# Kernel optimization log

Measured on AMD Instinct MI355X. Metric: run time of the kernel, lower is better.

## Reference

```python
import jax, jax.numpy as jnp
import numpy as np

B, S, E, D, A = 32, 2048, 1024, 1024, 1024


def setup_inputs() -> dict:
    key = jax.random.key(0)
    k1, k2, k3, k4, k5, k6, k7, k8 = jax.random.split(key, 8)
    # Kaiming-uniform-ish init scales (values don't matter for correctness)
    def lin(kw, kb, fan_in, fan_out):
        bound = 1.0 / np.sqrt(fan_in)
        W = jax.random.uniform(kw, (fan_out, fan_in), minval=-bound, maxval=bound, dtype=jnp.float32)
        b = jax.random.uniform(kb, (fan_out,), minval=-bound, maxval=bound, dtype=jnp.float32)
        return W, b
    W_enc, b_enc = lin(k1, k2, E, A)
    W_dec, b_dec = lin(k3, k4, D, A)
    W_v, b_v = lin(k5, k6, A, 1)
    encoder_out = jax.random.normal(k7, (B, S, E), dtype=jnp.float32)
    decoder_hidden = jax.random.normal(k8, (B, D), dtype=jnp.float32)
    return {
        "encoder_out": encoder_out,
        "decoder_hidden": decoder_hidden,
        "W_enc": W_enc, "b_enc": b_enc,
        "W_dec": W_dec, "b_dec": b_dec,
        "W_v": W_v, "b_v": b_v,
    }


def reference(encoder_out, decoder_hidden, W_enc, b_enc, W_dec, b_dec, W_v, b_v):
    # encoder_proj: [B, S, A]
    encoder_proj = jnp.einsum('bse,ae->bsa', encoder_out, W_enc) + b_enc
    # decoder_proj: [B, 1, A]
    decoder_proj = (jnp.einsum('bd,ad->ba', decoder_hidden, W_dec) + b_dec)[:, None, :]
    # scores: [B, S] (V projects attention_dim -> 1)
    scores = jnp.einsum('bsa,a->bs', jnp.tanh(encoder_proj + decoder_proj), W_v[0]) + b_v[0]
    alpha = jax.nn.softmax(scores, axis=1)  # [B, S]
    context = jnp.einsum('bse,bs->be', encoder_out, alpha)  # [B, E]
    return (context, alpha)
```

## Files before the change

### kernel.cpp

```cpp
#include <hip/hip_runtime.h>

typedef unsigned short ushort_t;
typedef __attribute__((ext_vector_type(8))) short short8;
typedef __attribute__((ext_vector_type(4))) float f32x4;


__device__ __forceinline__ ushort_t f2bf(float f) {
    unsigned u = __builtin_bit_cast(unsigned, f);
    u += 0x7fffu + ((u >> 16) & 1u);
    return (ushort_t)(u >> 16);
}

__device__ __forceinline__ float bf2f(ushort_t h) {
    unsigned u = ((unsigned)h) << 16;
    return __builtin_bit_cast(float, u);
}

__device__ __forceinline__ float tanh_fast(float x) {
    float e = __expf(2.0f * x);
    float r = __builtin_amdgcn_rcpf(e + 1.0f);
    return __builtin_fmaf(-2.0f, r, 1.0f);
}

__device__ __forceinline__ void gld16(const ushort_t* g, ushort_t* lds) {
    __builtin_amdgcn_global_load_lds(
        (const __attribute__((address_space(1))) unsigned int*)g,
        (__attribute__((address_space(3))) unsigned int*)lds, 16, 0, 0);
}


__global__ __launch_bounds__(256) void k_front(const float* __restrict__ enc,
                                               const float* __restrict__ Wenc,
                                               const float* __restrict__ dh,
                                               const float* __restrict__ Wd,
                                               const float* __restrict__ bd,
                                               const float* __restrict__ be,
                                               ushort_t* __restrict__ encB,
                                               ushort_t* __restrict__ wencB,
                                               float* __restrict__ dproj,
                                               float4* __restrict__ scores4) {
    const int bx = blockIdx.x;
    const int t = threadIdx.x;
    if (bx < 8192) {
        int i = bx * 256 + t;
        for (; i < 17055744; i += 2097152) {
            if (i < 16777216) {
                float4 v = ((const float4*)enc)[i];
                ushort4 o;
                o.x = f2bf(v.x); o.y = f2bf(v.y); o.z = f2bf(v.z); o.w = f2bf(v.w);
                ((ushort4*)encB)[i] = o;
            } else if (i < 17039360) {
                int j = i - 16777216;
                float4 v = ((const float4*)Wenc)[j];
                ushort4 o;
                o.x = f2bf(v.x); o.y = f2bf(v.y); o.z = f2bf(v.z); o.w = f2bf(v.w);
                ((ushort4*)wencB)[j] = o;
            } else {
                scores4[i - 17039360] = (float4){0.f, 0.f, 0.f, 0.f};
            }
        }
    } else {
        int wid = (bx - 8192) * 4 + (t >> 6);
        int lane = t & 63;
        int a = wid & 1023, b = wid >> 10;
        const float4* x = (const float4*)(dh + (size_t)b * 1024);
        const float4* wrow = (const float4*)(Wd + (size_t)a * 1024);
        float s = 0.f;
#pragma unroll
        for (int it = 0; it < 4; ++it) {
            int c = it * 64 + lane;
            float4 xv = x[c], wv = wrow[c];
            s += xv.x * wv.x + xv.y * wv.y + xv.z * wv.z + xv.w * wv.w;
        }
#pragma unroll
        for (int o = 1; o < 64; o <<= 1) s += __shfl_xor(s, o, 64);
        if (lane == 0) dproj[b * 1024 + a] = s + bd[a] + be[a];
    }
}


__global__ __launch_bounds__(256, 2) void k_gemm_scores(const ushort_t* __restrict__ A,
                                                        const ushort_t* __restrict__ Bm,
                                                        const float* __restrict__ dproj,
                                                        const float* __restrict__ Wv,
                                                        float* __restrict__ scores) {
    __shared__ __align__(16) ushort_t At[256 * 64];
    __shared__ __align__(16) ushort_t Bt[128 * 64];

    const int tid = threadIdx.x;
    const int lane = tid & 63;
    const int w = tid >> 6;
    const int wm = w >> 1, wn = w & 1;

    const int blk = blockIdx.x;
    const int q2 = blk >> 3;
    const int blkN = q2 & 7;
    const int blkM = (blk & 7) + ((q2 >> 3) << 3);
    const long long arow0 = (long long)blkM * 256;
    const int brow0 = blkN * 128;

    const int sr = lane >> 3;
    const int sgrp = lane & 7;
    const int c8s = sgrp ^ sr;

    const int q = lane >> 4;
    const int ml = lane & 15;

    const ushort_t* ga = A + (arow0 + w * 64 + sr) * 1024 + c8s * 8;
    const ushort_t* gb = Bm + (long long)(brow0 + w * 32 + sr) * 1024 + c8s * 8;

    f32x4 acc[8][4];
#pragma unroll
    for (int i = 0; i < 8; ++i)
#pragma unroll
        for (int jj = 0; jj < 4; ++jj) acc[i][jj] = (f32x4){0.f, 0.f, 0.f, 0.f};

    for (int k0 = 0; k0 < 1024; k0 += 64) {
        __syncthreads();
#pragma unroll
        for (int j = 0; j < 8; ++j)
            gld16(ga + j * 8192, &At[(w * 8 + j) * 512]);
#pragma unroll
        for (int j = 0; j < 4; ++j)
            gld16(gb + j * 8192, &Bt[(w * 4 + j) * 512]);
        ga += 64; gb += 64;
        __builtin_amdgcn_s_waitcnt(0);
        __syncthreads();

#pragma unroll
        for (int kk = 0; kk < 2; ++kk) {
            const int kb = kk * 4;
            const int slot = (kb + q) ^ (ml & 7);
            short8 af[8], bfr[4];
#pragma unroll
            for (int i = 0; i < 8; ++i) {
                int row = wm * 128 + i * 16 + ml;
                af[i] = *(const short8*)&At[row * 64 + slot * 8];
            }
#pragma unroll
            for (int jj = 0; jj < 4; ++jj) {
                int col = wn * 64 + jj * 16 + ml;
                bfr[jj] = *(const short8*)&Bt[col * 64 + slot * 8];
            }
#pragma unroll
            for (int i = 0; i < 8; ++i)
#pragma unroll
                for (int jj = 0; jj < 4; ++jj)
                    acc[i][jj] = __builtin_amdgcn_mfma_f32_16x16x32_bf16(
                        af[i], bfr[jj], acc[i][jj], 0, 0, 0);
        }
    }

    const int bb = blkM >> 3;
    float dp[4], wv[4];
#pragma unroll
    for (int jj = 0; jj < 4; ++jj) {
        int a = blkN * 128 + wn * 64 + jj * 16 + ml;
        dp[jj] = dproj[bb * 1024 + a];
        wv[jj] = Wv[a];
    }
#pragma unroll
    for (int i = 0; i < 8; ++i) {
        float rs[4] = {0.f, 0.f, 0.f, 0.f};
#pragma unroll
        for (int jj = 0; jj < 4; ++jj) {
            f32x4 v = acc[i][jj];
            rs[0] += wv[jj] * tanh_fast(v.x + dp[jj]);
            rs[1] += wv[jj] * tanh_fast(v.y + dp[jj]);
            rs[2] += wv[jj] * tanh_fast(v.z + dp[jj]);
            rs[3] += wv[jj] * tanh_fast(v.w + dp[jj]);
        }
#pragma unroll
        for (int r = 0; r < 4; ++r)
#pragma unroll
            for (int o = 1; o < 16; o <<= 1) rs[r] += __shfl_xor(rs[r], o, 64);
        if (ml == 0) {
            long long m0 = arow0 + wm * 128 + i * 16 + q * 4;
            atomicAdd(&scores[m0 + 0], rs[0]);
            atomicAdd(&scores[m0 + 1], rs[1]);
            atomicAdd(&scores[m0 + 2], rs[2]);
            atomicAdd(&scores[m0 + 3], rs[3]);
        }
    }
}


__global__ __launch_bounds__(256) void k_softmax(const float* __restrict__ scores,
                                                 float* __restrict__ out) {
    const int b = blockIdx.x, t = threadIdx.x;
    const int lane = t & 63, w = t >> 6;
    __shared__ float red[4];
#pragma unroll
    for (int j = t; j < 1024; j += 256) out[b * 1024 + j] = 0.f;
    float v[8];
#pragma unroll
    for (int j = 0; j < 8; ++j) v[j] = scores[b * 2048 + j * 256 + t];
    float mx = v[0];
#pragma unroll
    for (int j = 1; j < 8; ++j) mx = fmaxf(mx, v[j]);
#pragma unroll
    for (int o = 1; o < 64; o <<= 1) mx = fmaxf(mx, __shfl_xor(mx, o, 64));
    if (lane == 0) red[w] = mx;
    __syncthreads();
    mx = fmaxf(fmaxf(red[0], red[1]), fmaxf(red[2], red[3]));
    float s = 0.f;
#pragma unroll
    for (int j = 0; j < 8; ++j) { v[j] = __expf(v[j] - mx); s += v[j]; }
#pragma unroll
    for (int o = 1; o < 64; o <<= 1) s += __shfl_xor(s, o, 64);
    __syncthreads();
    if (lane == 0) red[w] = s;
    __syncthreads();
    s = red[0] + red[1] + red[2] + red[3];
    float inv = 1.0f / s;
#pragma unroll
    for (int j = 0; j < 8; ++j) out[32768 + b * 2048 + j * 256 + t] = v[j] * inv;
}


__global__ __launch_bounds__(256) void k_context(const ushort_t* __restrict__ encB,
                                                 const float* __restrict__ alpha,
                                                 float* __restrict__ out) {
    const int b = blockIdx.x, ec = blockIdx.y, sc = blockIdx.z, t = threadIdx.x;
    const int l = t & 31, g = t >> 5;
    __shared__ float al[256];
    __shared__ f32x4 part[8][33];
    al[t] = alpha[b * 2048 + sc * 256 + t];
    __syncthreads();
    const ushort_t* ep = encB + ((size_t)(b * 2048 + sc * 256 + g * 32)) * 1024 + ec * 128 + l * 4;
    const float* ag = &al[g * 32];
    f32x4 acc = (f32x4){0.f, 0.f, 0.f, 0.f};
#pragma unroll 4
    for (int s = 0; s < 32; ++s) {
        ushort4 ev = *(const ushort4*)(ep + (size_t)s * 1024);
        float a = ag[s];
        acc.x += a * bf2f(ev.x);
        acc.y += a * bf2f(ev.y);
        acc.z += a * bf2f(ev.z);
        acc.w += a * bf2f(ev.w);
    }
    part[g][l] = acc;
    __syncthreads();
    if (t < 32) {
        f32x4 s = part[0][t];
#pragma unroll
        for (int gg = 1; gg < 8; ++gg) {
            f32x4 p = part[gg][t];
            s.x += p.x; s.y += p.y; s.z += p.z; s.w += p.w;
        }
        float* dst = out + b * 1024 + ec * 128 + t * 4;
        atomicAdd(dst + 0, s.x);
        atomicAdd(dst + 1, s.y);
        atomicAdd(dst + 2, s.z);
        atomicAdd(dst + 3, s.w);
    }
}


extern "C" void kernel_launch(void* const* d_in, const int* in_sizes, int n_in,
                              void* d_out, int out_size, void* d_ws, size_t ws_size,
                              hipStream_t stream) {
    const float* enc  = (const float*)d_in[0];
    const float* dh   = (const float*)d_in[1];
    const float* Wenc = (const float*)d_in[2];
    const float* benc = (const float*)d_in[3];
    const float* Wdec = (const float*)d_in[4];
    const float* bdec = (const float*)d_in[5];
    const float* Wv   = (const float*)d_in[6];
    float* out = (float*)d_out;

    char* ws = (char*)d_ws;
    ushort_t* encB  = (ushort_t*)ws;
    ushort_t* wencB = (ushort_t*)(ws + 134217728ull);
    float* dproj    = (float*)(ws + 134217728ull + 2097152ull);
    float* scores   = (float*)(ws + 134217728ull + 2097152ull + 131072ull);

    k_front<<<16384, 256, 0, stream>>>(enc, Wenc, dh, Wdec, bdec, benc,
                                       encB, wencB, dproj, (float4*)scores);
    k_gemm_scores<<<2048, 256, 0, stream>>>(encB, wencB, dproj, Wv, scores);
    k_softmax<<<32, 256, 0, stream>>>(scores, out);
    k_context<<<dim3(32, 8, 8), 256, 0, stream>>>(encB, out + 32768, out);
}
```

Before: 552.7 us.

## Convert encoder activations to bf16 inside GEMM instead of separate pass

The standalone fp32-to-bf16 conversion of the 256MB encoder tensor is removed. The GEMM now loads fp32 rows directly, packs them to bf16 with v_cvt_pk_bf16_f32 in registers and stores them into LDS, in place of the async global_load_lds for A. The context kernel reads fp32 encoder data directly, with one block per (batch, E-chunk) covering the full sequence, so the output no longer needs atomics or zeroing. This avoids writing and re-reading a 128MB bf16 copy. In exchange the GEMM moves twice the bytes per A tile through registers, and the context kernel reads fp32.

Measured after the change: 608.5 us. +10.1%, slower.

```diff
diff --git a/kernel.cpp b/kernel.cpp
--- a/kernel.cpp
+++ b/kernel.cpp
@@ -3,6 +3,7 @@
 typedef unsigned short ushort_t;
 typedef __attribute__((ext_vector_type(8))) short short8;
 typedef __attribute__((ext_vector_type(4))) float f32x4;
+typedef __attribute__((ext_vector_type(4))) unsigned int u32x4;
 
 
 __device__ __forceinline__ ushort_t f2bf(float f) {
@@ -11,9 +12,10 @@
     return (ushort_t)(u >> 16);
 }
 
-__device__ __forceinline__ float bf2f(ushort_t h) {
-    unsigned u = ((unsigned)h) << 16;
-    return __builtin_bit_cast(float, u);
+__device__ __forceinline__ unsigned pkbf(float a, float b) {
+    unsigned r;
+    asm("v_cvt_pk_bf16_f32 %0, %1, %2" : "=v"(r) : "v"(a), "v"(b));
+    return r;
 }
 
 __device__ __forceinline__ float tanh_fast(float x) {
@@ -29,38 +31,29 @@
 }
 
 
-__global__ __launch_bounds__(256) void k_front(const float* __restrict__ enc,
-                                               const float* __restrict__ Wenc,
-                                               const float* __restrict__ dh,
-                                               const float* __restrict__ Wd,
-                                               const float* __restrict__ bd,
-                                               const float* __restrict__ be,
-                                               ushort_t* __restrict__ encB,
-                                               ushort_t* __restrict__ wencB,
-                                               float* __restrict__ dproj,
-                                               float4* __restrict__ scores4) {
+__global__ __launch_bounds__(256) void k_prep(const float* __restrict__ Wenc,
+                                              const float* __restrict__ dh,
+                                              const float* __restrict__ Wd,
+                                              const float* __restrict__ bd,
+                                              const float* __restrict__ be,
+                                              ushort_t* __restrict__ wencB,
+                                              float* __restrict__ dproj,
+                                              float4* __restrict__ scores4) {
     const int bx = blockIdx.x;
     const int t = threadIdx.x;
-    if (bx < 8192) {
-        int i = bx * 256 + t;
-        for (; i < 17055744; i += 2097152) {
-            if (i < 16777216) {
-                float4 v = ((const float4*)enc)[i];
-                ushort4 o;
-                o.x = f2bf(v.x); o.y = f2bf(v.y); o.z = f2bf(v.z); o.w = f2bf(v.w);
-                ((ushort4*)encB)[i] = o;
-            } else if (i < 17039360) {
-                int j = i - 16777216;
-                float4 v = ((const float4*)Wenc)[j];
-                ushort4 o;
-                o.x = f2bf(v.x); o.y = f2bf(v.y); o.z = f2bf(v.z); o.w = f2bf(v.w);
-                ((ushort4*)wencB)[j] = o;
-            } else {
-                scores4[i - 17039360] = (float4){0.f, 0.f, 0.f, 0.f};
-            }
-        }
+    if (bx < 256) {
+        int idx = bx * 256 + t;
+#pragma unroll
+        for (int r = 0; r < 4; ++r) {
+            int i = idx + r * 65536;
+            float4 v = ((const float4*)Wenc)[i];
+            ushort4 o;
+            o.x = f2bf(v.x); o.y = f2bf(v.y); o.z = f2bf(v.z); o.w = f2bf(v.w);
+            ((ushort4*)wencB)[i] = o;
+        }
+        if (idx < 16384) scores4[idx] = (float4){0.f, 0.f, 0.f, 0.f};
     } else {
-        int wid = (bx - 8192) * 4 + (t >> 6);
+        int wid = (bx - 256) * 4 + (t >> 6);
         int lane = t & 63;
         int a = wid & 1023, b = wid >> 10;
         const float4* x = (const float4*)(dh + (size_t)b * 1024);
@@ -79,7 +72,7 @@
 }
 
 
-__global__ __launch_bounds__(256, 2) void k_gemm_scores(const ushort_t* __restrict__ A,
+__global__ __launch_bounds__(256, 2) void k_gemm_scores(const float* __restrict__ A,
                                                         const ushort_t* __restrict__ Bm,
                                                         const float* __restrict__ dproj,
                                                         const float* __restrict__ Wv,
@@ -106,8 +99,9 @@
     const int q = lane >> 4;
     const int ml = lane & 15;
 
-    const ushort_t* ga = A + (arow0 + w * 64 + sr) * 1024 + c8s * 8;
-    const ushort_t* gb = Bm + (long long)(brow0 + w * 32 + sr) * 1024 + c8s * 8;
+    const float4* ga = (const float4*)(A + (size_t)(arow0 + w * 64 + sr) * 1024) + sgrp * 2;
+    const ushort_t* gb = Bm + (size_t)(brow0 + w * 32 + sr) * 1024 + c8s * 8;
+    const int wls = sr * 64 + (c8s << 3);
 
     f32x4 acc[8][4];
 #pragma unroll
@@ -116,14 +110,29 @@
         for (int jj = 0; jj < 4; ++jj) acc[i][jj] = (f32x4){0.f, 0.f, 0.f, 0.f};
 
     for (int k0 = 0; k0 < 1024; k0 += 64) {
+        float4 p0[4], p1[4];
+#pragma unroll
+        for (int j = 0; j < 4; ++j) { p0[j] = ga[j * 2048]; p1[j] = ga[j * 2048 + 1]; }
         __syncthreads();
-#pragma unroll
-        for (int j = 0; j < 8; ++j)
-            gld16(ga + j * 8192, &At[(w * 8 + j) * 512]);
 #pragma unroll
         for (int j = 0; j < 4; ++j)
             gld16(gb + j * 8192, &Bt[(w * 4 + j) * 512]);
-        ga += 64; gb += 64;
+#pragma unroll
+        for (int j = 0; j < 4; ++j) {
+            u32x4 o;
+            o.x = pkbf(p0[j].x, p0[j].y); o.y = pkbf(p0[j].z, p0[j].w);
+            o.z = pkbf(p1[j].x, p1[j].y); o.w = pkbf(p1[j].z, p1[j].w);
+            *(u32x4*)&At[(w * 8 + j) * 512 + wls] = o;
+        }
+#pragma unroll
+        for (int j = 4; j < 8; ++j) {
+            float4 v0 = ga[j * 2048], v1 = ga[j * 2048 + 1];
+            u32x4 o;
+            o.x = pkbf(v0.x, v0.y); o.y = pkbf(v0.z, v0.w);
+            o.z = pkbf(v1.x, v1.y); o.w = pkbf(v1.z, v1.w);
+            *(u32x4*)&At[(w * 8 + j) * 512 + wls] = o;
+        }
+        ga += 16; gb += 64;
         __builtin_amdgcn_s_waitcnt(0);
         __syncthreads();
 
@@ -186,12 +195,10 @@
 
 
 __global__ __launch_bounds__(256) void k_softmax(const float* __restrict__ scores,
-                                                 float* __restrict__ out) {
+                                                 float* __restrict__ alpha) {
     const int b = blockIdx.x, t = threadIdx.x;
     const int lane = t & 63, w = t >> 6;
     __shared__ float red[4];
-#pragma unroll
-    for (int j = t; j < 1024; j += 256) out[b * 1024 + j] = 0.f;
     float v[8];
 #pragma unroll
     for (int j = 0; j < 8; ++j) v[j] = scores[b * 2048 + j * 256 + t];
@@ -214,45 +221,42 @@
     s = red[0] + red[1] + red[2] + red[3];
     float inv = 1.0f / s;
 #pragma unroll
-    for (int j = 0; j < 8; ++j) out[32768 + b * 2048 + j * 256 + t] = v[j] * inv;
-}
-
-
-__global__ __launch_bounds__(256) void k_context(const ushort_t* __restrict__ encB,
+    for (int j = 0; j < 8; ++j) alpha[b * 2048 + j * 256 + t] = v[j] * inv;
+}
+
+
+__global__ __launch_bounds__(512) void k_context(const float* __restrict__ enc,
                                                  const float* __restrict__ alpha,
                                                  float* __restrict__ out) {
-    const int b = blockIdx.x, ec = blockIdx.y, sc = blockIdx.z, t = threadIdx.x;
+    const int b = blockIdx.x, ec = blockIdx.y;
+    const int t = threadIdx.x;
     const int l = t & 31, g = t >> 5;
-    __shared__ float al[256];
-    __shared__ f32x4 part[8][33];
-    al[t] = alpha[b * 2048 + sc * 256 + t];
-    __syncthreads();
-    const ushort_t* ep = encB + ((size_t)(b * 2048 + sc * 256 + g * 32)) * 1024 + ec * 128 + l * 4;
-    const float* ag = &al[g * 32];
+    __shared__ float al[2048];
+    __shared__ f32x4 part[16][33];
+    for (int j = t; j < 2048; j += 512) al[j] = alpha[b * 2048 + j];
+    __syncthreads();
+    const float4* ep = (const float4*)enc + ((size_t)b * 2048 + g) * 256 + ec * 32 + l;
     f32x4 acc = (f32x4){0.f, 0.f, 0.f, 0.f};
-#pragma unroll 4
-    for (int s = 0; s < 32; ++s) {
-        ushort4 ev = *(const ushort4*)(ep + (size_t)s * 1024);
-        float a = ag[s];
-        acc.x += a * bf2f(ev.x);
-        acc.y += a * bf2f(ev.y);
-        acc.z += a * bf2f(ev.z);
-        acc.w += a * bf2f(ev.w);
+#pragma unroll 8
+    for (int it = 0; it < 128; ++it) {
+        float4 v = ep[(size_t)it * 4096];
+        float a = al[g + it * 16];
+        acc.x += a * v.x;
+        acc.y += a * v.y;
+        acc.z += a * v.z;
+        acc.w += a * v.w;
     }
     part[g][l] = acc;
     __syncthreads();
     if (t < 32) {
         f32x4 s = part[0][t];
 #pragma unroll
-        for (int gg = 1; gg < 8; ++gg) {
+        for (int gg = 1; gg < 16; ++gg) {
             f32x4 p = part[gg][t];
             s.x += p.x; s.y += p.y; s.z += p.z; s.w += p.w;
         }
-        float* dst = out + b * 1024 + ec * 128 + t * 4;
-        atomicAdd(dst + 0, s.x);
-        atomicAdd(dst + 1, s.y);
-        atomicAdd(dst + 2, s.z);
-        atomicAdd(dst + 3, s.w);
+        *(float4*)(out + (size_t)b * 1024 + ec * 128 + t * 4) =
+            (float4){s.x, s.y, s.z, s.w};
     }
 }
 
@@ -270,14 +274,13 @@
     float* out = (float*)d_out;
 
     char* ws = (char*)d_ws;
-    ushort_t* encB  = (ushort_t*)ws;
-    ushort_t* wencB = (ushort_t*)(ws + 134217728ull);
-    float* dproj    = (float*)(ws + 134217728ull + 2097152ull);
-    float* scores   = (float*)(ws + 134217728ull + 2097152ull + 131072ull);
-
-    k_front<<<16384, 256, 0, stream>>>(enc, Wenc, dh, Wdec, bdec, benc,
-                                       encB, wencB, dproj, (float4*)scores);
-    k_gemm_scores<<<2048, 256, 0, stream>>>(encB, wencB, dproj, Wv, scores);
-    k_softmax<<<32, 256, 0, stream>>>(scores, out);
-    k_context<<<dim3(32, 8, 8), 256, 0, stream>>>(encB, out + 32768, out);
-}
+    ushort_t* wencB = (ushort_t*)ws;
+    float* dproj    = (float*)(ws + 2097152ull);
+    float* scores   = (float*)(ws + 2097152ull + 131072ull);
+
+    k_prep<<<8448, 256, 0, stream>>>(Wenc, dh, Wdec, bdec, benc,
+                                     wencB, dproj, (float4*)scores);
+    k_gemm_scores<<<2048, 256, 0, stream>>>(enc, wencB, dproj, Wv, scores);
+    k_softmax<<<32, 256, 0, stream>>>(scores, out + 32768);
+    k_context<<<dim3(32, 8), 512, 0, stream>>>(enc, out + 32768, out);
+}
```

## Fuse softmax into context kernel and drop atomic accumulation

Applied to the files above, without the earlier changes.

Merges the softmax and context kernels into one kernel: each of 32x8 blocks recomputes the full softmax over the batch row, stores alpha in LDS, and one block per batch writes alpha to the output. Each block now covers all 2048 sequence positions for its 128-column slice, so the context result is written directly instead of through atomics, and the output no longer needs zero-initialising. This removes one launch and the atomic traffic, but cuts the grid from 2048 blocks to 256, which lowers parallelism for streaming the 128MB bf16 encoder copy.

After: 545.9 us. No clear change (-1.2%).

```diff
diff --git a/kernel.cpp b/kernel.cpp
--- a/kernel.cpp
+++ b/kernel.cpp
@@ -185,55 +185,49 @@
 }
 
 
-__global__ __launch_bounds__(256) void k_softmax(const float* __restrict__ scores,
-                                                 float* __restrict__ out) {
-    const int b = blockIdx.x, t = threadIdx.x;
-    const int lane = t & 63, w = t >> 6;
-    __shared__ float red[4];
-#pragma unroll
-    for (int j = t; j < 1024; j += 256) out[b * 1024 + j] = 0.f;
-    float v[8];
-#pragma unroll
-    for (int j = 0; j < 8; ++j) v[j] = scores[b * 2048 + j * 256 + t];
-    float mx = v[0];
-#pragma unroll
-    for (int j = 1; j < 8; ++j) mx = fmaxf(mx, v[j]);
+__global__ __launch_bounds__(512) void k_ctx(const ushort_t* __restrict__ encB,
+                                             const float* __restrict__ scores,
+                                             float* __restrict__ out) {
+    const int b = blockIdx.x, ec = blockIdx.y;
+    const int t = threadIdx.x;
+    const int l = t & 31, g = t >> 5;
+    const int lane = t & 63, wv = t >> 6;
+    __shared__ float al[2048];
+    __shared__ float red[8];
+    __shared__ f32x4 part[16][33];
+
+    float4 v = ((const float4*)scores)[b * 512 + t];
+    float mx = fmaxf(fmaxf(v.x, v.y), fmaxf(v.z, v.w));
 #pragma unroll
     for (int o = 1; o < 64; o <<= 1) mx = fmaxf(mx, __shfl_xor(mx, o, 64));
-    if (lane == 0) red[w] = mx;
-    __syncthreads();
-    mx = fmaxf(fmaxf(red[0], red[1]), fmaxf(red[2], red[3]));
-    float s = 0.f;
-#pragma unroll
-    for (int j = 0; j < 8; ++j) { v[j] = __expf(v[j] - mx); s += v[j]; }
+    if (lane == 0) red[wv] = mx;
+    __syncthreads();
+    mx = red[0];
+#pragma unroll
+    for (int j = 1; j < 8; ++j) mx = fmaxf(mx, red[j]);
+    float e0 = __expf(v.x - mx), e1 = __expf(v.y - mx);
+    float e2 = __expf(v.z - mx), e3 = __expf(v.w - mx);
+    float s = e0 + e1 + e2 + e3;
 #pragma unroll
     for (int o = 1; o < 64; o <<= 1) s += __shfl_xor(s, o, 64);
     __syncthreads();
-    if (lane == 0) red[w] = s;
-    __syncthreads();
-    s = red[0] + red[1] + red[2] + red[3];
+    if (lane == 0) red[wv] = s;
+    __syncthreads();
+    s = 0.f;
+#pragma unroll
+    for (int j = 0; j < 8; ++j) s += red[j];
     float inv = 1.0f / s;
-#pragma unroll
-    for (int j = 0; j < 8; ++j) out[32768 + b * 2048 + j * 256 + t] = v[j] * inv;
-}
-
-
-__global__ __launch_bounds__(256) void k_context(const ushort_t* __restrict__ encB,
-                                                 const float* __restrict__ alpha,
-                                                 float* __restrict__ out) {
-    const int b = blockIdx.x, ec = blockIdx.y, sc = blockIdx.z, t = threadIdx.x;
-    const int l = t & 31, g = t >> 5;
-    __shared__ float al[256];
-    __shared__ f32x4 part[8][33];
-    al[t] = alpha[b * 2048 + sc * 256 + t];
-    __syncthreads();
-    const ushort_t* ep = encB + ((size_t)(b * 2048 + sc * 256 + g * 32)) * 1024 + ec * 128 + l * 4;
-    const float* ag = &al[g * 32];
+    float4 a4 = (float4){e0 * inv, e1 * inv, e2 * inv, e3 * inv};
+    ((float4*)al)[t] = a4;
+    if (ec == 0) ((float4*)(out + 32768 + (size_t)b * 2048))[t] = a4;
+    __syncthreads();
+
+    const ushort_t* ep = encB + ((size_t)b * 2048 + g) * 1024 + ec * 128 + l * 4;
     f32x4 acc = (f32x4){0.f, 0.f, 0.f, 0.f};
-#pragma unroll 4
-    for (int s = 0; s < 32; ++s) {
-        ushort4 ev = *(const ushort4*)(ep + (size_t)s * 1024);
-        float a = ag[s];
+#pragma unroll 8
+    for (int it = 0; it < 128; ++it) {
+        ushort4 ev = *(const ushort4*)(ep + (size_t)it * 16384);
+        float a = al[g + it * 16];
         acc.x += a * bf2f(ev.x);
         acc.y += a * bf2f(ev.y);
         acc.z += a * bf2f(ev.z);
@@ -242,17 +236,14 @@
     part[g][l] = acc;
     __syncthreads();
     if (t < 32) {
-        f32x4 s = part[0][t];
-#pragma unroll
-        for (int gg = 1; gg < 8; ++gg) {
-            f32x4 p = part[gg][t];
-            s.x += p.x; s.y += p.y; s.z += p.z; s.w += p.w;
-        }
-        float* dst = out + b * 1024 + ec * 128 + t * 4;
-        atomicAdd(dst + 0, s.x);
-        atomicAdd(dst + 1, s.y);
-        atomicAdd(dst + 2, s.z);
-        atomicAdd(dst + 3, s.w);
+        f32x4 ss = part[0][t];
+#pragma unroll
+        for (int gg = 1; gg < 16; ++gg) {
+            f32x4 pp = part[gg][t];
+            ss.x += pp.x; ss.y += pp.y; ss.z += pp.z; ss.w += pp.w;
+        }
+        *(float4*)(out + (size_t)b * 1024 + ec * 128 + t * 4) =
+            (float4){ss.x, ss.y, ss.z, ss.w};
     }
 }
 
@@ -278,6 +269,5 @@
     k_front<<<16384, 256, 0, stream>>>(enc, Wenc, dh, Wdec, bdec, benc,
                                        encB, wencB, dproj, (float4*)scores);
     k_gemm_scores<<<2048, 256, 0, stream>>>(encB, wencB, dproj, Wv, scores);
-    k_softmax<<<32, 256, 0, stream>>>(scores, out);
-    k_context<<<dim3(32, 8, 8), 256, 0, stream>>>(encB, out + 32768, out);
-}
+    k_ctx<<<dim3(32, 8), 512, 0, stream>>>(encB, scores, out);
+}
```
